# Kernel tuning notes

Hardware: AMD Instinct MI355X
Metric: run time of the kernel (lower is better)

The kernel has to match this reference:

```python
import jax, jax.numpy as jnp
import numpy as np


def setup_inputs() -> dict:
    key = jax.random.key(0)
    k1, k2 = jax.random.split(key)
    d = 1024
    seq_len = 32768
    hidden = jax.random.normal(k1, (d,), dtype=jnp.float32)
    encoder_outputs = jax.random.normal(k2, (seq_len, d), dtype=jnp.float32)
    return {"hidden": hidden, "encoder_outputs": encoder_outputs}


def reference(hidden, encoder_outputs):
    # Original: per-timestep python loop of hidden.dot(encoder_outputs[i]),
    # then sigmoid, then unsqueeze twice -> [1, 1, seq_len].
    # Vectorized as a single matvec: scores[s] = sum_d E[s,d] * h[d].
    scores = jnp.einsum('sd,d->s', encoder_outputs, hidden)  # [seq_len]
    return jax.nn.sigmoid(scores)[None, None, :]  # [1, 1, seq_len]
```

## Files before the change

### kernel.cpp

```cpp
#include <hip/hip_runtime.h>
#include <hip/hip_bf16.h>
#include <math.h>

__global__ void attn_matvec_sigmoid(const float* __restrict__ h,
                                    const float* __restrict__ E,
                                    float* __restrict__ out,
                                    int seq_len, int d) {
    const int waves_per_block = blockDim.x >> 6;
    const int wave = blockIdx.x * waves_per_block + (threadIdx.x >> 6);
    const int lane = threadIdx.x & 63;
    if (wave >= seq_len) return;

    const float4* __restrict__ row = reinterpret_cast<const float4*>(E + (size_t)wave * d);
    const float4* __restrict__ hv  = reinterpret_cast<const float4*>(h);

    const int nvec = d >> 2;
    float acc = 0.0f;
#pragma unroll 4
    for (int i = lane; i < nvec; i += 64) {
        float4 e = row[i];
        float4 hh = hv[i];
        acc += e.x * hh.x + e.y * hh.y + e.z * hh.z + e.w * hh.w;
    }

#pragma unroll
    for (int off = 32; off > 0; off >>= 1)
        acc += __shfl_xor(acc, off, 64);

    if (lane == 0)
        out[wave] = 1.0f / (1.0f + __expf(-acc));
}

extern "C" void kernel_launch(void* const* d_in, const int* in_sizes, int n_in,
                              void* d_out, int out_size, void* d_ws, size_t ws_size,
                              hipStream_t stream) {
    const float* hidden = (const float*)d_in[0];
    const float* enc    = (const float*)d_in[1];
    float* out          = (float*)d_out;

    const int d = in_sizes[0];
    const int seq_len = out_size;

    const int block = 256;
    const int waves_per_block = block / 64;
    const int grid = (seq_len + waves_per_block - 1) / waves_per_block;

    attn_matvec_sigmoid<<<grid, block, 0, stream>>>(hidden, enc, out, seq_len, d);
}
```

Measured before the change: 24.49 us.

## Process four rows per wave with hidden vector held in registers

Each wave now computes four output rows. The hidden vector is loaded once into registers, and all 16 float4 loads of E are issued before any compute so more memory requests are in flight. The four reductions are interleaved and the four sigmoid results go out in a single float4 store. The kernel hardcodes d=1024 and assumes seq_len is a multiple of 4, and it raises register use.

New measurement: 26.23 us. 1.07x slower.

```diff
diff --git a/kernel.cpp b/kernel.cpp
--- a/kernel.cpp
+++ b/kernel.cpp
@@ -2,33 +2,64 @@
 #include <hip/hip_bf16.h>
 #include <math.h>
 
-__global__ void attn_matvec_sigmoid(const float* __restrict__ h,
-                                    const float* __restrict__ E,
-                                    float* __restrict__ out,
-                                    int seq_len, int d) {
+
+__device__ __forceinline__ float dot4(float4 a, float4 b) {
+    return a.x * b.x + a.y * b.y + a.z * b.z + a.w * b.w;
+}
+
+__global__ __launch_bounds__(256) void attn_matvec_sigmoid4(
+        const float* __restrict__ h,
+        const float* __restrict__ E,
+        float* __restrict__ out,
+        int seq_len, int d) {
     const int waves_per_block = blockDim.x >> 6;
     const int wave = blockIdx.x * waves_per_block + (threadIdx.x >> 6);
     const int lane = threadIdx.x & 63;
-    if (wave >= seq_len) return;
+    const int total_waves = gridDim.x * waves_per_block;
 
-    const float4* __restrict__ row = reinterpret_cast<const float4*>(E + (size_t)wave * d);
-    const float4* __restrict__ hv  = reinterpret_cast<const float4*>(h);
+    const float4* __restrict__ hv = reinterpret_cast<const float4*>(h);
+    const float4 h0 = hv[lane];
+    const float4 h1 = hv[lane + 64];
+    const float4 h2 = hv[lane + 128];
+    const float4 h3 = hv[lane + 192];
 
-    const int nvec = d >> 2;
-    float acc = 0.0f;
-#pragma unroll 4
-    for (int i = lane; i < nvec; i += 64) {
-        float4 e = row[i];
-        float4 hh = hv[i];
-        acc += e.x * hh.x + e.y * hh.y + e.z * hh.z + e.w * hh.w;
-    }
+    const int nvec_row = d >> 2;
+
+    for (int base = wave * 4; base < seq_len; base += total_waves * 4) {
+        float acc0 = 0.f, acc1 = 0.f, acc2 = 0.f, acc3 = 0.f;
+
+        const float4* r0 = reinterpret_cast<const float4*>(E + (size_t)(base + 0) * d);
+        const float4* r1 = reinterpret_cast<const float4*>(E + (size_t)(base + 1) * d);
+        const float4* r2 = reinterpret_cast<const float4*>(E + (size_t)(base + 2) * d);
+        const float4* r3 = reinterpret_cast<const float4*>(E + (size_t)(base + 3) * d);
+
+        float4 a0 = r0[lane],       b0 = r1[lane],       c0 = r2[lane],       e0 = r3[lane];
+        float4 a1 = r0[lane + 64],  b1 = r1[lane + 64],  c1 = r2[lane + 64],  e1 = r3[lane + 64];
+        float4 a2 = r0[lane + 128], b2 = r1[lane + 128], c2 = r2[lane + 128], e2 = r3[lane + 128];
+        float4 a3 = r0[lane + 192], b3 = r1[lane + 192], c3 = r2[lane + 192], e3 = r3[lane + 192];
+
+        acc0 = dot4(a0, h0) + dot4(a1, h1) + dot4(a2, h2) + dot4(a3, h3);
+        acc1 = dot4(b0, h0) + dot4(b1, h1) + dot4(b2, h2) + dot4(b3, h3);
+        acc2 = dot4(c0, h0) + dot4(c1, h1) + dot4(c2, h2) + dot4(c3, h3);
+        acc3 = dot4(e0, h0) + dot4(e1, h1) + dot4(e2, h2) + dot4(e3, h3);
 
 #pragma unroll
-    for (int off = 32; off > 0; off >>= 1)
-        acc += __shfl_xor(acc, off, 64);
+        for (int off = 32; off > 0; off >>= 1) {
+            acc0 += __shfl_xor(acc0, off, 64);
+            acc1 += __shfl_xor(acc1, off, 64);
+            acc2 += __shfl_xor(acc2, off, 64);
+            acc3 += __shfl_xor(acc3, off, 64);
+        }
 
-    if (lane == 0)
-        out[wave] = 1.0f / (1.0f + __expf(-acc));
+        if (lane == 0) {
+            float4 o;
+            o.x = 1.0f / (1.0f + __expf(-acc0));
+            o.y = 1.0f / (1.0f + __expf(-acc1));
+            o.z = 1.0f / (1.0f + __expf(-acc2));
+            o.w = 1.0f / (1.0f + __expf(-acc3));
+            *reinterpret_cast<float4*>(out + base) = o;
+        }
+    }
 }
 
 extern "C" void kernel_launch(void* const* d_in, const int* in_sizes, int n_in,
@@ -43,7 +74,9 @@
 
     const int block = 256;
     const int waves_per_block = block / 64;
-    const int grid = (seq_len + waves_per_block - 1) / waves_per_block;
+    const int rows_per_wave = 4;
+    int waves_needed = (seq_len + rows_per_wave - 1) / rows_per_wave;
+    int grid = (waves_needed + waves_per_block - 1) / waves_per_block;
 
-    attn_matvec_sigmoid<<<grid, block, 0, stream>>>(hidden, enc, out, seq_len, d);
+    attn_matvec_sigmoid4<<<grid, block, 0, stream>>>(hidden, enc, out, seq_len, d);
 }
```

## Use persistent grid-stride waves with register-cached hidden vector for d=1024

Applied to the files above, without the earlier changes.

Each wave now loads the hidden vector once into registers (four float4 per lane) and processes multiple rows in a grid-stride loop over a fixed grid of 2048 blocks. It removes the per-row reload of the hidden vector and block scheduling overhead. Launch bounds are added to allow 8 blocks per CU. The code hardcodes d=1024 (four float4 per lane), so other hidden sizes would give wrong results.

Result: slower. 24.98 us (+2.0%).

```diff
diff --git a/kernel.cpp b/kernel.cpp
--- a/kernel.cpp
+++ b/kernel.cpp
@@ -2,33 +2,43 @@
 #include <hip/hip_bf16.h>
 #include <math.h>
 
-__global__ void attn_matvec_sigmoid(const float* __restrict__ h,
-                                    const float* __restrict__ E,
-                                    float* __restrict__ out,
-                                    int seq_len, int d) {
-    const int waves_per_block = blockDim.x >> 6;
-    const int wave = blockIdx.x * waves_per_block + (threadIdx.x >> 6);
+
+__device__ __forceinline__ float dot4(float4 a, float4 b) {
+    return a.x * b.x + a.y * b.y + a.z * b.z + a.w * b.w;
+}
+
+__global__ __launch_bounds__(256, 8) void attn_matvec_sigmoid_p(
+        const float* __restrict__ h,
+        const float* __restrict__ E,
+        float* __restrict__ out,
+        int seq_len, int d) {
     const int lane = threadIdx.x & 63;
-    if (wave >= seq_len) return;
+    const int wave = blockIdx.x * (blockDim.x >> 6) + (threadIdx.x >> 6);
+    const int total_waves = gridDim.x * (blockDim.x >> 6);
 
-    const float4* __restrict__ row = reinterpret_cast<const float4*>(E + (size_t)wave * d);
-    const float4* __restrict__ hv  = reinterpret_cast<const float4*>(h);
+    const float4* __restrict__ hv = reinterpret_cast<const float4*>(h);
+    const float4 h0 = hv[lane];
+    const float4 h1 = hv[lane + 64];
+    const float4 h2 = hv[lane + 128];
+    const float4 h3 = hv[lane + 192];
 
-    const int nvec = d >> 2;
-    float acc = 0.0f;
-#pragma unroll 4
-    for (int i = lane; i < nvec; i += 64) {
-        float4 e = row[i];
-        float4 hh = hv[i];
-        acc += e.x * hh.x + e.y * hh.y + e.z * hh.z + e.w * hh.w;
-    }
+    for (int row = wave; row < seq_len; row += total_waves) {
+        const float4* __restrict__ r =
+            reinterpret_cast<const float4*>(E + (size_t)row * d);
+        float4 a0 = r[lane];
+        float4 a1 = r[lane + 64];
+        float4 a2 = r[lane + 128];
+        float4 a3 = r[lane + 192];
+
+        float acc = dot4(a0, h0) + dot4(a1, h1) + dot4(a2, h2) + dot4(a3, h3);
 
 #pragma unroll
-    for (int off = 32; off > 0; off >>= 1)
-        acc += __shfl_xor(acc, off, 64);
+        for (int off = 32; off > 0; off >>= 1)
+            acc += __shfl_xor(acc, off, 64);
 
-    if (lane == 0)
-        out[wave] = 1.0f / (1.0f + __expf(-acc));
+        if (lane == 0)
+            out[row] = 1.0f / (1.0f + __expf(-acc));
+    }
 }
 
 extern "C" void kernel_launch(void* const* d_in, const int* in_sizes, int n_in,
@@ -42,8 +52,7 @@
     const int seq_len = out_size;
 
     const int block = 256;
-    const int waves_per_block = block / 64;
-    const int grid = (seq_len + waves_per_block - 1) / waves_per_block;
+    const int grid = 2048;
 
-    attn_matvec_sigmoid<<<grid, block, 0, stream>>>(hidden, enc, out, seq_len, d);
+    attn_matvec_sigmoid_p<<<grid, block, 0, stream>>>(hidden, enc, out, seq_len, d);
 }
```
